# Kernel tuning notes

Hardware: AMD Instinct MI355X
Metric: run time of the kernel (lower is better)

Reference implementation:

```python
import jax, jax.numpy as jnp
import numpy as np

N, E, B, DIM, NF, EF, HID = 16384, 32768, 512, 64, 14, 4, 128

def _p(key, shape, scale):
    return jax.random.normal(key, shape, dtype=jnp.float32) * scale

def setup_inputs() -> dict:
    key = jax.random.key(0)
    ks = jax.random.split(key, 20)
    s = lambda fan: 1.0 / float(np.sqrt(fan))
    z = lambda *sh: jnp.zeros(sh, jnp.float32)
    return {
        "x": jax.random.normal(ks[0], (N, NF), dtype=jnp.float32),
        "edge_index": jax.random.randint(ks[1], (2, E), 0, N),
        "edge_attr": jax.random.uniform(ks[2], (E, EF), dtype=jnp.float32),
        "batch": jnp.sort(jax.random.randint(ks[3], (N,), 0, B)),
        "do_dropout": 0,
        "mlp_drop": 0,
        "lin0_w": _p(ks[4], (NF, DIM), s(NF)), "lin0_b": z(DIM),
        "nn1_w": _p(ks[5], (EF, HID), s(EF)), "nn1_b": z(HID),
        "nn2_w": _p(ks[6], (HID, DIM * DIM), s(HID)), "nn2_b": z(DIM * DIM),
        "root_w": _p(ks[7], (DIM, DIM), s(DIM)), "conv_b": z(DIM),
        "gru_w_ih": _p(ks[8], (3 * DIM, DIM), s(DIM)), "gru_w_hh": _p(ks[9], (3 * DIM, DIM), s(DIM)),
        "gru_b_ih": _p(ks[10], (3 * DIM,), s(DIM)), "gru_b_hh": _p(ks[11], (3 * DIM,), s(DIM)),
        "lstm_w_ih": _p(ks[12], (4 * DIM, 2 * DIM), s(DIM)), "lstm_w_hh": _p(ks[13], (4 * DIM, DIM), s(DIM)),
        "lstm_b_ih": _p(ks[14], (4 * DIM,), s(DIM)), "lstm_b_hh": _p(ks[15], (4 * DIM,), s(DIM)),
        "lin1_w": _p(ks[16], (2 * DIM, DIM), s(2 * DIM)), "lin1_b": z(DIM),
        "lin2_w": _p(ks[17], (DIM, 1), s(DIM)), "lin2_b": z(1),
    }

def _forward(x, edge_attr, lin0_w, lin0_b, nn1_w, nn1_b, nn2_w, nn2_b, root_w, conv_b,
             gru_w_ih, gru_w_hh, gru_b_ih, gru_b_hh,
             lstm_w_ih, lstm_w_hh, lstm_b_ih, lstm_b_hh,
             lin1_w, lin1_b, lin2_w, lin2_b, edge_index, batch):
    src, dst = edge_index[0], edge_index[1]
    out = jax.nn.relu(x @ lin0_w + lin0_b)                      # [N, DIM]
    h = out
    # Edge-conditioned weights (edge_attr is layer-independent -> compute once)
    ew = jax.nn.relu(edge_attr @ nn1_w + nn1_b) @ nn2_w + nn2_b  # [E, DIM*DIM]
    ew = ew.reshape(E, DIM, DIM)
    deg = jax.ops.segment_sum(jnp.ones((E,), jnp.float32), dst, num_segments=N)
    deg = jnp.maximum(deg, 1.0)[:, None]                        # mean aggregation denominator

    def gru_cell(xin, hprev):
        gi = xin @ gru_w_ih.T + gru_b_ih
        gh = hprev @ gru_w_hh.T + gru_b_hh
        ir, iz, inn = jnp.split(gi, 3, axis=-1)
        hr, hz, hn = jnp.split(gh, 3, axis=-1)
        r = jax.nn.sigmoid(ir + hr)
        zg = jax.nn.sigmoid(iz + hz)
        n = jnp.tanh(inn + r * hn)
        return (1.0 - zg) * n + zg * hprev

    for _ in range(3):  # 3 message-passing rounds (structurally fixed)
        msg = jnp.einsum('ed,edf->ef', out[src], ew)            # gather -> per-edge matvec
        agg = jax.ops.segment_sum(msg, dst, num_segments=N) / deg
        m = jax.nn.relu(out @ root_w + agg + conv_b)            # NNConv (root weight + mean aggr)
        h = gru_cell(m, h)
        out = h

    # Set2Set pooling, 3 processing steps
    q_star = jnp.zeros((B, 2 * DIM), jnp.float32)
    hl = jnp.zeros((B, DIM), jnp.float32)
    cl = jnp.zeros((B, DIM), jnp.float32)
    for _ in range(3):
        gates = q_star @ lstm_w_ih.T + lstm_b_ih + hl @ lstm_w_hh.T + lstm_b_hh
        ii, ff, gg, oo = jnp.split(gates, 4, axis=-1)
        cl = jax.nn.sigmoid(ff) * cl + jax.nn.sigmoid(ii) * jnp.tanh(gg)
        hl = jax.nn.sigmoid(oo) * jnp.tanh(cl)
        q = hl                                                  # [B, DIM]
        e = jnp.sum(out * q[batch], axis=-1)                    # [N]
        emax = jax.ops.segment_max(e, batch, num_segments=B)
        ex = jnp.exp(e - emax[batch])
        esum = jnp.maximum(jax.ops.segment_sum(ex, batch, num_segments=B), 1e-16)
        a = ex / esum[batch]                                    # segment softmax
        r = jax.ops.segment_sum(a[:, None] * out, batch, num_segments=B)
        q_star = jnp.concatenate([q, r], axis=-1)               # [B, 2*DIM]

    y = jax.nn.relu(q_star @ lin1_w + lin1_b)
    # dropout flags are False (eval) -> identity
    y = y @ lin2_w + lin2_b
    return y.reshape(-1)                                        # [B]

def reference(x, edge_index, edge_attr, batch, do_dropout, mlp_drop,
              lin0_w, lin0_b, nn1_w, nn1_b, nn2_w, nn2_b, root_w, conv_b,
              gru_w_ih, gru_w_hh, gru_b_ih, gru_b_hh,
              lstm_w_ih, lstm_w_hh, lstm_b_ih, lstm_b_hh,
              lin1_w, lin1_b, lin2_w, lin2_b):
    return _forward(x, edge_attr, lin0_w, lin0_b, nn1_w, nn1_b, nn2_w, nn2_b, root_w, conv_b,
                    gru_w_ih, gru_w_hh, gru_b_ih, gru_b_hh,
                    lstm_w_ih, lstm_w_hh, lstm_b_ih, lstm_b_hh,
                    lin1_w, lin1_b, lin2_w, lin2_b, edge_index, batch)
```

## Files before the change

### kernel.cpp

```cpp
#include <hip/hip_runtime.h>
#include <math.h>

#define N_NODES 16384
#define N_EDGES 32768
#define NGRAPH  512
#define DIM     64
#define NF      14
#define HIDN    128
#define EWCOLS  4096

typedef unsigned short u16;
typedef unsigned int   u32;
typedef __attribute__((ext_vector_type(8))) short bf16x8;
typedef __attribute__((ext_vector_type(4))) float f32x4;
typedef __attribute__((ext_vector_type(4))) u32   u32x4;

__device__ inline float b2f(u16 u){
    unsigned int x = ((unsigned int)u) << 16;
    return __builtin_bit_cast(float, x);
}
__device__ inline u16 f2b(float f){
    unsigned int x = __builtin_bit_cast(unsigned int, f);
    unsigned int r = (x + 0x7FFFu + ((x >> 16) & 1u)) >> 16;
    return (u16)r;
}
__device__ inline float sigf(float x){ return 1.f / (1.f + expf(-x)); }

__global__ __launch_bounds__(256) void k_lin0(const float* __restrict__ x,
        const float* __restrict__ w, const float* __restrict__ b, float* __restrict__ out){
    int n = (blockIdx.x * blockDim.x + threadIdx.x) >> 6;
    int lane = threadIdx.x & 63;
    if (n >= N_NODES) return;
    float xv = (lane < NF) ? x[n * NF + lane] : 0.f;
    float acc = b[lane];
    #pragma unroll
    for (int d = 0; d < NF; ++d){
        float xd = __shfl(xv, d);
        acc += xd * w[d * DIM + lane];
    }
    out[n * DIM + lane] = fmaxf(acc, 0.f);
}

__global__ __launch_bounds__(256) void k_prep(const float* __restrict__ w2,
        const float* __restrict__ lwih, const float* __restrict__ lwhh,
        const float* __restrict__ root, const float* __restrict__ gwih, const float* __restrict__ gwhh,
        u16* __restrict__ w2T, float* __restrict__ wihT, float* __restrict__ whhT,
        u16* __restrict__ rtHi, u16* __restrict__ rtLo,
        u16* __restrict__ wihHi, u16* __restrict__ wihLo,
        u16* __restrict__ whhHi, u16* __restrict__ whhLo){
    int i = blockIdx.x * 256 + threadIdx.x;
    if (i < 524288){
        int k = i >> 12, c = i & 4095;
        w2T[c * HIDN + k] = f2b(w2[i]);
    } else if (i < 557056){
        int i2 = i - 524288;
        int j = i2 >> 7, d = i2 & 127;
        wihT[d * 256 + j] = lwih[i2];
    } else if (i < 573440){
        int i2 = i - 557056;
        int j = i2 >> 6, d = i2 & 63;
        whhT[d * 256 + j] = lwhh[i2];
    } else if (i < 577536){
        int i2 = i - 573440;
        int d = i2 >> 6, j = i2 & 63;
        float v = root[i2]; u16 h = f2b(v);
        rtHi[j * 64 + d] = h; rtLo[j * 64 + d] = f2b(v - b2f(h));
    } else if (i < 589824){
        int k = i - 577536;
        float v = gwih[k]; u16 h = f2b(v);
        wihHi[k] = h; wihLo[k] = f2b(v - b2f(h));
    } else if (i < 602112){
        int k = i - 589824;
        float v = gwhh[k]; u16 h = f2b(v);
        whhHi[k] = h; whhLo[k] = f2b(v - b2f(h));
    }
}

__global__ __launch_bounds__(256) void k_deg(const int* __restrict__ ei, unsigned* __restrict__ degu){
    int e = blockIdx.x * blockDim.x + threadIdx.x;
    if (e < N_EDGES) atomicAdd(&degu[ei[N_EDGES + e]], 1u);
}
__global__ __launch_bounds__(256) void k_dinv(const unsigned* __restrict__ degu, float* __restrict__ dinv){
    int n = blockIdx.x * blockDim.x + threadIdx.x;
    if (n < N_NODES) dinv[n] = 1.f / fmaxf((float)degu[n], 1.f);
}

#define EB   128
#define LDO  68

__global__ __launch_bounds__(512) void k_msg_fused(
        const int* __restrict__ ei, const float* __restrict__ ea,
        const float* __restrict__ w1, const float* __restrict__ b1,
        const u16* __restrict__ w2T, const float* __restrict__ b2,
        const float* __restrict__ out, float* __restrict__ agg)
{
    __shared__ float s_out[EB * LDO];
    __shared__ u16   s_b[2][64 * 128];
    __shared__ float s_b2[EWCOLS];
    __shared__ float s_w1[512];
    __shared__ float s_b1[128];
    int tid = threadIdx.x;
    int e0 = blockIdx.x * EB;

    s_w1[tid] = w1[tid];
    if (tid < 128) s_b1[tid] = b1[tid];
    {
        int base = tid * 8;
        *(float4*)(s_b2 + base)     = *(const float4*)(b2 + base);
        *(float4*)(s_b2 + base + 4) = *(const float4*)(b2 + base + 4);
    }
    {
        int row = tid >> 2, cb = (tid & 3) * 16;
        int s = ei[e0 + row];
        const float4* sp = (const float4*)(out + (size_t)s * DIM + cb);
        float4 v0 = sp[0], v1 = sp[1], v2 = sp[2], v3 = sp[3];
        float* dst = s_out + row * LDO + cb;
        *(float4*)(dst)      = v0;
        *(float4*)(dst + 4)  = v1;
        *(float4*)(dst + 8)  = v2;
        *(float4*)(dst + 12) = v3;
    }
    __syncthreads();

    int wv = tid >> 6, lane = tid & 63;
    int WR = (wv >> 1) * 32, WC = (wv & 1) * 32;
    int lr = lane & 15, lk = (lane >> 4) * 8;

    bf16x8 afr[2][4];
    #pragma unroll
    for (int m = 0; m < 2; ++m){
        int erow = e0 + WR + m*16 + lr;
        float4 av = *(const float4*)(ea + (size_t)erow * 4);
        #pragma unroll
        for (int kk = 0; kk < 4; ++kk){
            bf16x8 t8;
            #pragma unroll
            for (int i = 0; i < 8; ++i){
                int h = kk*32 + lk + i;
                float acc = s_b1[h] + av.x*s_w1[h] + av.y*s_w1[128+h]
                          + av.z*s_w1[256+h] + av.w*s_w1[384+h];
                t8[i] = (short)f2b(fmaxf(acc, 0.f));
            }
            afr[m][kk] = t8;
        }
    }

    int bc = tid >> 3, bs = tid & 7;
    const u32x4* gb = (const u32x4*)w2T;
    u32x4 r0 = gb[((size_t)bc << 4) + bs*2];
    u32x4 r1 = gb[((size_t)bc << 4) + bs*2 + 1];

    f32x4 msg[2][2] = {};
    int swzr = (lr & 7) << 4;
    int swzw = (bc & 7) << 4;
    int crow = (lane >> 4) * 4;

    for (int d = 0; d < 64; ++d){
        char* sw = (char*)s_b[d & 1];
        *(u32x4*)(sw + ((bc*256 + bs*32)      ^ swzw)) = r0;
        *(u32x4*)(sw + ((bc*256 + bs*32 + 16) ^ swzw)) = r1;
        if (d < 63){
            size_t base = ((size_t)(d+1)*64 + bc) << 4;
            r0 = gb[base + bs*2];
            r1 = gb[base + bs*2 + 1];
        }
        __syncthreads();
        const char* sr = (const char*)s_b[d & 1];
        f32x4 ew[2][2] = {};
        #pragma unroll
        for (int kk = 0; kk < 4; ++kk){
            int kb = kk*64 + (lane >> 4) * 16;
            bf16x8 bf0 = *(const bf16x8*)(sr + (((WC + lr)*256 + kb)      ^ swzr));
            bf16x8 bf1 = *(const bf16x8*)(sr + (((WC + 16 + lr)*256 + kb) ^ swzr));
            ew[0][0] = __builtin_amdgcn_mfma_f32_16x16x32_bf16(afr[0][kk], bf0, ew[0][0], 0, 0, 0);
            ew[0][1] = __builtin_amdgcn_mfma_f32_16x16x32_bf16(afr[0][kk], bf1, ew[0][1], 0, 0, 0);
            ew[1][0] = __builtin_amdgcn_mfma_f32_16x16x32_bf16(afr[1][kk], bf0, ew[1][0], 0, 0, 0);
            ew[1][1] = __builtin_amdgcn_mfma_f32_16x16x32_bf16(afr[1][kk], bf1, ew[1][1], 0, 0, 0);
        }
        float b2v0 = s_b2[d*64 + WC + lr];
        float b2v1 = s_b2[d*64 + WC + 16 + lr];
        #pragma unroll
        for (int m = 0; m < 2; ++m){
            #pragma unroll
            for (int r = 0; r < 4; ++r){
                float sc = s_out[(WR + m*16 + crow + r) * LDO + d];
                msg[m][0][r] += sc * (ew[m][0][r] + b2v0);
                msg[m][1][r] += sc * (ew[m][1][r] + b2v1);
            }
        }
    }

    #pragma unroll
    for (int m = 0; m < 2; ++m){
        #pragma unroll
        for (int r = 0; r < 4; ++r){
            int eg = e0 + WR + m*16 + crow + r;
            int dn = ei[N_EDGES + eg];
            atomicAdd(&agg[(size_t)dn * DIM + WC + lr],      msg[m][0][r]);
            atomicAdd(&agg[(size_t)dn * DIM + WC + 16 + lr], msg[m][1][r]);
        }
    }
}

#define LDH 68
__global__ __launch_bounds__(256) void k_update(
        const u16* __restrict__ rtHi, const u16* __restrict__ rtLo,
        const u16* __restrict__ wihHi, const u16* __restrict__ wihLo,
        const u16* __restrict__ whhHi, const u16* __restrict__ whhLo,
        const float* __restrict__ convb, const float* __restrict__ bih,
        const float* __restrict__ bhh,
        const float* __restrict__ agg, const float* __restrict__ dinv,
        float* __restrict__ out)
{
    __shared__ float s_h[64 * LDH];
    __shared__ float s_aux[64 * LDH];
    __shared__ float s_m[64 * LDH];
    int tid = threadIdx.x;
    int n0 = blockIdx.x * 64;

    {
        int row = tid >> 2, cb = (tid & 3) * 16;
        const float4* hp = (const float4*)(out + (size_t)(n0 + row) * DIM + cb);
        const float4* ap = (const float4*)(agg + (size_t)(n0 + row) * DIM + cb);
        float di = dinv[n0 + row];
        #pragma unroll
        for (int q = 0; q < 4; ++q){
            float4 hv = hp[q];
            float4 av = ap[q];
            *(float4*)(s_h + row * LDH + cb + q*4) = hv;
            float4 xv;
            xv.x = av.x * di + convb[cb + q*4 + 0];
            xv.y = av.y * di + convb[cb + q*4 + 1];
            xv.z = av.z * di + convb[cb + q*4 + 2];
            xv.w = av.w * di + convb[cb + q*4 + 3];
            *(float4*)(s_aux + row * LDH + cb + q*4) = xv;
        }
    }
    __syncthreads();

    int wv = tid >> 6, lane = tid & 63;
    int lr = lane & 15, lkb = (lane >> 4) * 8;
    int arow = wv * 16 + lr;

    bf16x8 hHi[2], hLo[2];
    #pragma unroll
    for (int kk = 0; kk < 2; ++kk){
        const float* src = s_h + arow * LDH + kk*32 + lkb;
        bf16x8 hi8, lo8;
        #pragma unroll
        for (int e = 0; e < 8; ++e){
            float v = src[e];
            u16 h = f2b(v);
            hi8[e] = (short)h;
            lo8[e] = (short)f2b(v - b2f(h));
        }
        hHi[kk] = hi8; hLo[kk] = lo8;
    }

    f32x4 c1[4] = {};
    #pragma unroll
    for (int ct = 0; ct < 4; ++ct){
        #pragma unroll
        for (int kk = 0; kk < 2; ++kk){
            int off = (ct*16 + lr) * 64 + kk*32 + lkb;
            bf16x8 bHi = *(const bf16x8*)(rtHi + off);
            bf16x8 bLo = *(const bf16x8*)(rtLo + off);
            c1[ct] = __builtin_amdgcn_mfma_f32_16x16x32_bf16(hHi[kk], bHi, c1[ct], 0, 0, 0);
            c1[ct] = __builtin_amdgcn_mfma_f32_16x16x32_bf16(hLo[kk], bHi, c1[ct], 0, 0, 0);
            c1[ct] = __builtin_amdgcn_mfma_f32_16x16x32_bf16(hHi[kk], bLo, c1[ct], 0, 0, 0);
        }
    }

    int crow = (lane >> 4) * 4;
    #pragma unroll
    for (int ct = 0; ct < 4; ++ct){
        #pragma unroll
        for (int r = 0; r < 4; ++r){
            int row = wv*16 + crow + r;
            int col = ct*16 + lr;
            float m = fmaxf(c1[ct][r] + s_aux[row * LDH + col], 0.f);
            s_m[row * LDH + col] = m;
        }
    }
    __syncthreads();

    bf16x8 mHi[2], mLo[2];
    #pragma unroll
    for (int kk = 0; kk < 2; ++kk){
        const float* src = s_m + arow * LDH + kk*32 + lkb;
        bf16x8 hi8, lo8;
        #pragma unroll
        for (int e = 0; e < 8; ++e){
            float v = src[e];
            u16 h = f2b(v);
            hi8[e] = (short)h;
            lo8[e] = (short)f2b(v - b2f(h));
        }
        mHi[kk] = hi8; mLo[kk] = lo8;
    }

    f32x4 gi[12] = {}, gh[12] = {};
    #pragma unroll
    for (int ct = 0; ct < 12; ++ct){
        #pragma unroll
        for (int kk = 0; kk < 2; ++kk){
            int off = (ct*16 + lr) * 64 + kk*32 + lkb;
            bf16x8 biH = *(const bf16x8*)(wihHi + off);
            bf16x8 biL = *(const bf16x8*)(wihLo + off);
            gi[ct] = __builtin_amdgcn_mfma_f32_16x16x32_bf16(mHi[kk], biH, gi[ct], 0, 0, 0);
            gi[ct] = __builtin_amdgcn_mfma_f32_16x16x32_bf16(mLo[kk], biH, gi[ct], 0, 0, 0);
            gi[ct] = __builtin_amdgcn_mfma_f32_16x16x32_bf16(mHi[kk], biL, gi[ct], 0, 0, 0);
            bf16x8 bhH = *(const bf16x8*)(whhHi + off);
            bf16x8 bhL = *(const bf16x8*)(whhLo + off);
            gh[ct] = __builtin_amdgcn_mfma_f32_16x16x32_bf16(hHi[kk], bhH, gh[ct], 0, 0, 0);
            gh[ct] = __builtin_amdgcn_mfma_f32_16x16x32_bf16(hLo[kk], bhH, gh[ct], 0, 0, 0);
            gh[ct] = __builtin_amdgcn_mfma_f32_16x16x32_bf16(hHi[kk], bhL, gh[ct], 0, 0, 0);
        }
    }

    #pragma unroll
    for (int ct = 0; ct < 4; ++ct){
        int col = ct*16 + lr;
        float br_i = bih[col],       br_h = bhh[col];
        float bz_i = bih[64 + col],  bz_h = bhh[64 + col];
        float bn_i = bih[128 + col], bn_h = bhh[128 + col];
        #pragma unroll
        for (int r = 0; r < 4; ++r){
            int row = wv*16 + crow + r;
            float rg = sigf(gi[ct][r] + br_i + gh[ct][r] + br_h);
            float zg = sigf(gi[ct+4][r] + bz_i + gh[ct+4][r] + bz_h);
            float ng = tanhf(gi[ct+8][r] + bn_i + rg * (gh[ct+8][r] + bn_h));
            float h  = s_h[row * LDH + col];
            s_aux[row * LDH + col] = (1.f - zg) * ng + zg * h;
        }
    }
    __syncthreads();

    {
        int row = tid >> 2, cb = (tid & 3) * 16;
        #pragma unroll
        for (int q = 0; q < 4; ++q)
            *(float4*)(out + (size_t)(n0 + row) * DIM + cb + q*4) =
                *(const float4*)(s_aux + row * LDH + cb + q*4);
    }
}

__global__ __launch_bounds__(256) void k_s2s(
        const float* __restrict__ out, const int* __restrict__ batch,
        const float* __restrict__ wihT, const float* __restrict__ lbih,
        const float* __restrict__ whhT, const float* __restrict__ lbhh,
        const float* __restrict__ l1w, const float* __restrict__ l1b,
        const float* __restrict__ l2w, const float* __restrict__ l2b,
        float* __restrict__ y)
{
    __shared__ float s_q[128];
    __shared__ float s_hc[128];
    __shared__ float s_g[256];
    __shared__ float s_rw[256];
    __shared__ float s_sw[8];
    __shared__ int   s_rng[2];
    int g = blockIdx.x, tid = threadIdx.x;
    if (tid < 2){
        int target = g + tid;
        int lo = 0, hi = N_NODES;
        while (lo < hi){ int mid = (lo + hi) >> 1; if (batch[mid] < target) lo = mid + 1; else hi = mid; }
        s_rng[tid] = lo;
    }
    if (tid < 128){ s_q[tid] = 0.f; s_hc[tid] = 0.f; }
    __syncthreads();
    int s0 = s_rng[0], s1 = s_rng[1];
    int wv = tid >> 6, lane = tid & 63;

    for (int step = 0; step < 3; ++step){
        float acc = lbih[tid] + lbhh[tid];
        #pragma unroll 8
        for (int d = 0; d < 128; ++d) acc += s_q[d] * wihT[d * 256 + tid];
        #pragma unroll 8
        for (int d = 0; d < 64;  ++d) acc += s_hc[d] * whhT[d * 256 + tid];
        s_g[tid] = acc;
        __syncthreads();
        if (tid < 64){
            float c = sigf(s_g[64 + tid]) * s_hc[64 + tid] + sigf(s_g[tid]) * tanhf(s_g[128 + tid]);
            float h = sigf(s_g[192 + tid]) * tanhf(c);
            s_hc[tid] = h; s_hc[64 + tid] = c;
            s_q[tid] = h;
        }
        __syncthreads();
        float q = s_hc[lane];
        float emx = -3.4e38f;
        for (int n = s0 + wv; n < s1; n += 4){
            float v = out[(size_t)n * DIM + lane] * q;
            #pragma unroll
            for (int off = 32; off; off >>= 1) v += __shfl_xor(v, off);
            emx = fmaxf(emx, v);
        }
        if (lane == 0) s_sw[wv] = emx;
        __syncthreads();
        float gmax = fmaxf(fmaxf(s_sw[0], s_sw[1]), fmaxf(s_sw[2], s_sw[3]));
        float rl = 0.f, ss = 0.f;
        for (int n = s0 + wv; n < s1; n += 4){
            float o = out[(size_t)n * DIM + lane];
            float v = o * q;
            #pragma unroll
            for (int off = 32; off; off >>= 1) v += __shfl_xor(v, off);
            float ex = expf(v - gmax);
            rl += ex * o;
            ss += ex;
        }
        s_rw[wv * 64 + lane] = rl;
        if (lane == 0) s_sw[4 + wv] = ss;
        __syncthreads();
        if (tid < 64){
            float r = s_rw[tid] + s_rw[64 + tid] + s_rw[128 + tid] + s_rw[192 + tid];
            float S = fmaxf(s_sw[4] + s_sw[5] + s_sw[6] + s_sw[7], 1e-16f);
            s_q[64 + tid] = r / S;
        }
        __syncthreads();
    }
    if (wv == 0){
        float acc = l1b[lane];
        #pragma unroll 8
        for (int d = 0; d < 128; ++d) acc += s_q[d] * l1w[d * 64 + lane];
        float h = fmaxf(acc, 0.f);
        float p = h * l2w[lane];
        #pragma unroll
        for (int off = 32; off; off >>= 1) p += __shfl_down(p, off);
        if (lane == 0) y[g] = p + l2b[0];
    }
}

extern "C" void kernel_launch(void* const* d_in, const int* in_sizes, int n_in,
                              void* d_out, int out_size, void* d_ws, size_t ws_size,
                              hipStream_t stream){
    const float* x      = (const float*)d_in[0];
    const int*   ei     = (const int*)d_in[1];
    const float* ea     = (const float*)d_in[2];
    const int*   batch  = (const int*)d_in[3];
    const float* lin0_w = (const float*)d_in[6];
    const float* lin0_b = (const float*)d_in[7];
    const float* nn1_w  = (const float*)d_in[8];
    const float* nn1_b  = (const float*)d_in[9];
    const float* nn2_w  = (const float*)d_in[10];
    const float* nn2_b  = (const float*)d_in[11];
    const float* root_w = (const float*)d_in[12];
    const float* conv_b = (const float*)d_in[13];
    const float* gwih   = (const float*)d_in[14];
    const float* gwhh   = (const float*)d_in[15];
    const float* gbih   = (const float*)d_in[16];
    const float* gbhh   = (const float*)d_in[17];
    const float* lwih   = (const float*)d_in[18];
    const float* lwhh   = (const float*)d_in[19];
    const float* lbih   = (const float*)d_in[20];
    const float* lbhh   = (const float*)d_in[21];
    const float* l1w    = (const float*)d_in[22];
    const float* l1b    = (const float*)d_in[23];
    const float* l2w    = (const float*)d_in[24];
    const float* l2b    = (const float*)d_in[25];
    float* y = (float*)d_out;

    char* p = (char*)d_ws;
    float* out   = (float*)p;    p += (size_t)N_NODES * DIM * 4;
    float* agg   = (float*)p;    p += (size_t)N_NODES * DIM * 4;
    u16* w2T     = (u16*)p;      p += (size_t)EWCOLS * HIDN * 2;
    float* wihT  = (float*)p;    p += 128 * 256 * 4;
    float* whhT  = (float*)p;    p += 64 * 256 * 4;
    u16* rtHi    = (u16*)p;      p += 4096 * 2;
    u16* rtLo    = (u16*)p;      p += 4096 * 2;
    u16* wihHi   = (u16*)p;      p += 12288 * 2;
    u16* wihLo   = (u16*)p;      p += 12288 * 2;
    u16* whhHi   = (u16*)p;      p += 12288 * 2;
    u16* whhLo   = (u16*)p;      p += 12288 * 2;
    unsigned* degu = (unsigned*)p; p += N_NODES * 4;
    float* dinv  = (float*)p;    p += N_NODES * 4;

    if ((size_t)(p - (char*)d_ws) > ws_size) return;

    hipMemsetAsync(degu, 0, N_NODES * 4, stream);

    k_prep<<<2352, 256, 0, stream>>>(nn2_w, lwih, lwhh, root_w, gwih, gwhh,
                w2T, wihT, whhT, rtHi, rtLo, wihHi, wihLo, whhHi, whhLo);
    k_lin0<<<N_NODES / 4, 256, 0, stream>>>(x, lin0_w, lin0_b, out);
    k_deg <<<N_EDGES / 256, 256, 0, stream>>>(ei, degu);
    k_dinv<<<N_NODES / 256, 256, 0, stream>>>(degu, dinv);

    for (int r = 0; r < 3; ++r){
        hipMemsetAsync(agg, 0, (size_t)N_NODES * DIM * 4, stream);
        k_msg_fused<<<N_EDGES / EB, 512, 0, stream>>>(ei, ea, nn1_w, nn1_b, w2T, nn2_b, out, agg);
        k_update   <<<N_NODES / 64, 256, 0, stream>>>(rtHi, rtLo, wihHi, wihLo, whhHi, whhLo,
                        conv_b, gbih, gbhh, agg, dinv, out);
    }

    k_s2s<<<NGRAPH, 256, 0, stream>>>(out, batch, wihT, lbih, whhT, lbhh,
                l1w, l1b, l2w, l2b, y);
}
```

Baseline: 300.9 us.

## Stream edge-weight tiles via direct global-to-LDS loads and hoist bias term

The per-edge weight tile loads in the fused message kernel now use global_load_lds, which writes straight into double-buffered shared memory instead of staging through registers. This removes the register round trip and the explicit LDS stores, with a single barrier per step. The gathered node features are stored transposed so each step reads them as one vector load. The b2 bias contribution is moved out of the main loop into a separate pass that reads b2 from global memory, which removes the bias shared-memory buffer and its per-step adds. The risks are that correctness now depends on the placement and semantics of the async LDS loads, and that the transposed scalar stores may cause bank conflicts.

```diff
diff --git a/kernel.cpp b/kernel.cpp
--- a/kernel.cpp
+++ b/kernel.cpp
@@ -14,6 +14,8 @@
 typedef __attribute__((ext_vector_type(8))) short bf16x8;
 typedef __attribute__((ext_vector_type(4))) float f32x4;
 typedef __attribute__((ext_vector_type(4))) u32   u32x4;
+typedef __attribute__((address_space(1))) const u32 as1_u32;
+typedef __attribute__((address_space(3))) u32       as3_u32;
 
 __device__ inline float b2f(u16 u){
     unsigned int x = ((unsigned int)u) << 16;
@@ -86,7 +88,7 @@
 }
 
 #define EB   128
-#define LDO  68
+#define LDT_O 132
 
 __global__ __launch_bounds__(512) void k_msg_fused(
         const int* __restrict__ ei, const float* __restrict__ ea,
@@ -94,37 +96,45 @@
         const u16* __restrict__ w2T, const float* __restrict__ b2,
         const float* __restrict__ out, float* __restrict__ agg)
 {
-    __shared__ float s_out[EB * LDO];
+    __shared__ float s_oT[64 * LDT_O];
     __shared__ u16   s_b[2][64 * 128];
-    __shared__ float s_b2[EWCOLS];
     __shared__ float s_w1[512];
     __shared__ float s_b1[128];
     int tid = threadIdx.x;
     int e0 = blockIdx.x * EB;
+    int wv = tid >> 6, lane = tid & 63;
+
+    int c0 = (wv*2)     * 4 + (lane >> 4);
+    int c1 = (wv*2 + 1) * 4 + (lane >> 4);
+    int o0 = ((((lane & 15) << 4) ^ ((c0 & 7) << 4)) >> 1);
+    int o1 = ((((lane & 15) << 4) ^ ((c1 & 7) << 4)) >> 1);
+    const u16* g0 = w2T + c0 * HIDN + o0;
+    const u16* g1 = w2T + c1 * HIDN + o1;
+
+    __builtin_amdgcn_global_load_lds((as1_u32*)g0,
+        (as3_u32*)((char*)s_b[0] + (wv*2)*1024), 16, 0, 0);
+    __builtin_amdgcn_global_load_lds((as1_u32*)g1,
+        (as3_u32*)((char*)s_b[0] + (wv*2+1)*1024), 16, 0, 0);
 
     s_w1[tid] = w1[tid];
     if (tid < 128) s_b1[tid] = b1[tid];
     {
-        int base = tid * 8;
-        *(float4*)(s_b2 + base)     = *(const float4*)(b2 + base);
-        *(float4*)(s_b2 + base + 4) = *(const float4*)(b2 + base + 4);
-    }
-    {
-        int row = tid >> 2, cb = (tid & 3) * 16;
+        int row = tid >> 2, q = tid & 3;
         int s = ei[e0 + row];
-        const float4* sp = (const float4*)(out + (size_t)s * DIM + cb);
+        const float4* sp = (const float4*)(out + (size_t)s * DIM + q * 16);
         float4 v0 = sp[0], v1 = sp[1], v2 = sp[2], v3 = sp[3];
-        float* dst = s_out + row * LDO + cb;
-        *(float4*)(dst)      = v0;
-        *(float4*)(dst + 4)  = v1;
-        *(float4*)(dst + 8)  = v2;
-        *(float4*)(dst + 12) = v3;
+        float* op = s_oT + (q * 16) * LDT_O + row;
+        op[0*LDT_O]=v0.x;  op[1*LDT_O]=v0.y;  op[2*LDT_O]=v0.z;  op[3*LDT_O]=v0.w;
+        op[4*LDT_O]=v1.x;  op[5*LDT_O]=v1.y;  op[6*LDT_O]=v1.z;  op[7*LDT_O]=v1.w;
+        op[8*LDT_O]=v2.x;  op[9*LDT_O]=v2.y;  op[10*LDT_O]=v2.z; op[11*LDT_O]=v2.w;
+        op[12*LDT_O]=v3.x; op[13*LDT_O]=v3.y; op[14*LDT_O]=v3.z; op[15*LDT_O]=v3.w;
     }
     __syncthreads();
 
-    int wv = tid >> 6, lane = tid & 63;
     int WR = (wv >> 1) * 32, WC = (wv & 1) * 32;
     int lr = lane & 15, lk = (lane >> 4) * 8;
+    int crow = (lane >> 4) * 4;
+    int swzr = (lr & 7) << 4;
 
     bf16x8 afr[2][4];
     #pragma unroll
@@ -145,48 +155,54 @@
         }
     }
 
-    int bc = tid >> 3, bs = tid & 7;
-    const u32x4* gb = (const u32x4*)w2T;
-    u32x4 r0 = gb[((size_t)bc << 4) + bs*2];
-    u32x4 r1 = gb[((size_t)bc << 4) + bs*2 + 1];
-
     f32x4 msg[2][2] = {};
-    int swzr = (lr & 7) << 4;
-    int swzw = (bc & 7) << 4;
-    int crow = (lane >> 4) * 4;
 
     for (int d = 0; d < 64; ++d){
-        char* sw = (char*)s_b[d & 1];
-        *(u32x4*)(sw + ((bc*256 + bs*32)      ^ swzw)) = r0;
-        *(u32x4*)(sw + ((bc*256 + bs*32 + 16) ^ swzw)) = r1;
-        if (d < 63){
-            size_t base = ((size_t)(d+1)*64 + bc) << 4;
-            r0 = gb[base + bs*2];
-            r1 = gb[base + bs*2 + 1];
-        }
-        __syncthreads();
+        if (d + 1 < 64){
+            size_t pb = (size_t)(d + 1) * 8192;
+            char* dst = (char*)s_b[(d + 1) & 1];
+            __builtin_amdgcn_global_load_lds((as1_u32*)(g0 + pb),
+                (as3_u32*)(dst + (wv*2)*1024), 16, 0, 0);
+            __builtin_amdgcn_global_load_lds((as1_u32*)(g1 + pb),
+                (as3_u32*)(dst + (wv*2+1)*1024), 16, 0, 0);
+        }
         const char* sr = (const char*)s_b[d & 1];
-        f32x4 ew[2][2] = {};
+        f32x4 ew00 = {}, ew01 = {}, ew10 = {}, ew11 = {};
         #pragma unroll
         for (int kk = 0; kk < 4; ++kk){
             int kb = kk*64 + (lane >> 4) * 16;
             bf16x8 bf0 = *(const bf16x8*)(sr + (((WC + lr)*256 + kb)      ^ swzr));
             bf16x8 bf1 = *(const bf16x8*)(sr + (((WC + 16 + lr)*256 + kb) ^ swzr));
-            ew[0][0] = __builtin_amdgcn_mfma_f32_16x16x32_bf16(afr[0][kk], bf0, ew[0][0], 0, 0, 0);
-            ew[0][1] = __builtin_amdgcn_mfma_f32_16x16x32_bf16(afr[0][kk], bf1, ew[0][1], 0, 0, 0);
-            ew[1][0] = __builtin_amdgcn_mfma_f32_16x16x32_bf16(afr[1][kk], bf0, ew[1][0], 0, 0, 0);
-            ew[1][1] = __builtin_amdgcn_mfma_f32_16x16x32_bf16(afr[1][kk], bf1, ew[1][1], 0, 0, 0);
-        }
-        float b2v0 = s_b2[d*64 + WC + lr];
-        float b2v1 = s_b2[d*64 + WC + 16 + lr];
-        #pragma unroll
-        for (int m = 0; m < 2; ++m){
-            #pragma unroll
-            for (int r = 0; r < 4; ++r){
-                float sc = s_out[(WR + m*16 + crow + r) * LDO + d];
-                msg[m][0][r] += sc * (ew[m][0][r] + b2v0);
-                msg[m][1][r] += sc * (ew[m][1][r] + b2v1);
-            }
+            ew00 = __builtin_amdgcn_mfma_f32_16x16x32_bf16(afr[0][kk], bf0, ew00, 0, 0, 0);
+            ew01 = __builtin_amdgcn_mfma_f32_16x16x32_bf16(afr[0][kk], bf1, ew01, 0, 0, 0);
+            ew10 = __builtin_amdgcn_mfma_f32_16x16x32_bf16(afr[1][kk], bf0, ew10, 0, 0, 0);
+            ew11 = __builtin_amdgcn_mfma_f32_16x16x32_bf16(afr[1][kk], bf1, ew11, 0, 0, 0);
+        }
+        f32x4 sc0 = *(const f32x4*)(s_oT + d * LDT_O + WR + crow);
+        f32x4 sc1 = *(const f32x4*)(s_oT + d * LDT_O + WR + 16 + crow);
+        #pragma unroll
+        for (int r = 0; r < 4; ++r){
+            msg[0][0][r] += sc0[r] * ew00[r];
+            msg[0][1][r] += sc0[r] * ew01[r];
+            msg[1][0][r] += sc1[r] * ew10[r];
+            msg[1][1][r] += sc1[r] * ew11[r];
+        }
+        __syncthreads();
+    }
+
+    int f0 = WC + lr;
+    #pragma unroll 8
+    for (int dd = 0; dd < 64; ++dd){
+        float bv0 = b2[dd*64 + f0];
+        float bv1 = b2[dd*64 + f0 + 16];
+        f32x4 sc0 = *(const f32x4*)(s_oT + dd * LDT_O + WR + crow);
+        f32x4 sc1 = *(const f32x4*)(s_oT + dd * LDT_O + WR + 16 + crow);
+        #pragma unroll
+        for (int r = 0; r < 4; ++r){
+            msg[0][0][r] += sc0[r] * bv0;
+            msg[0][1][r] += sc0[r] * bv1;
+            msg[1][0][r] += sc1[r] * bv0;
+            msg[1][1][r] += sc1[r] * bv1;
         }
     }
 
```

Result: slower. 357.7 us (+18.9%).

## Split message kernel over input-dimension halves to raise occupancy

Applied to the files above, without the earlier changes.

The fused edge-message kernel now launches a second grid dimension, with each block handling 32 of the 64 input features (d) for its 128 edges, so grid size doubles from 256 to 512 blocks. Shared memory is shrunk by staging only half of each source row and by dropping the shared nn2 bias copy in favour of direct global loads, and launch bounds request 4 blocks per SM. The edge MLP hidden layer is recomputed in both halves and twice as many atomicAdds hit agg, trading redundant work and atomic traffic for better GPU fill on a small grid.

```diff
diff --git a/kernel.cpp b/kernel.cpp
--- a/kernel.cpp
+++ b/kernel.cpp
@@ -86,39 +86,37 @@
 }
 
 #define EB   128
-#define LDO  68
-
-__global__ __launch_bounds__(512) void k_msg_fused(
+#define LDO2 36
+
+__global__ __launch_bounds__(512, 4) void k_msg_fused(
         const int* __restrict__ ei, const float* __restrict__ ea,
         const float* __restrict__ w1, const float* __restrict__ b1,
         const u16* __restrict__ w2T, const float* __restrict__ b2,
         const float* __restrict__ out, float* __restrict__ agg)
 {
-    __shared__ float s_out[EB * LDO];
+    __shared__ float s_out[EB * LDO2];
     __shared__ u16   s_b[2][64 * 128];
-    __shared__ float s_b2[EWCOLS];
     __shared__ float s_w1[512];
     __shared__ float s_b1[128];
     int tid = threadIdx.x;
     int e0 = blockIdx.x * EB;
+    int d0 = blockIdx.y * 32;
+
+    int bc = tid >> 3, bs = tid & 7;
+    const u32x4* gb = (const u32x4*)w2T;
+    u32x4 r0 = gb[(((size_t)d0 * 64 + bc) << 4) + bs*2];
+    u32x4 r1 = gb[(((size_t)d0 * 64 + bc) << 4) + bs*2 + 1];
 
     s_w1[tid] = w1[tid];
     if (tid < 128) s_b1[tid] = b1[tid];
     {
-        int base = tid * 8;
-        *(float4*)(s_b2 + base)     = *(const float4*)(b2 + base);
-        *(float4*)(s_b2 + base + 4) = *(const float4*)(b2 + base + 4);
-    }
-    {
-        int row = tid >> 2, cb = (tid & 3) * 16;
+        int row = tid >> 2, q = tid & 3;
         int s = ei[e0 + row];
-        const float4* sp = (const float4*)(out + (size_t)s * DIM + cb);
-        float4 v0 = sp[0], v1 = sp[1], v2 = sp[2], v3 = sp[3];
-        float* dst = s_out + row * LDO + cb;
-        *(float4*)(dst)      = v0;
-        *(float4*)(dst + 4)  = v1;
-        *(float4*)(dst + 8)  = v2;
-        *(float4*)(dst + 12) = v3;
+        const float4* sp = (const float4*)(out + (size_t)s * DIM + d0 + q * 8);
+        float4 v0 = sp[0], v1 = sp[1];
+        float* dst = s_out + row * LDO2 + q * 8;
+        *(float4*)(dst)     = v0;
+        *(float4*)(dst + 4) = v1;
     }
     __syncthreads();
 
@@ -145,48 +143,44 @@
         }
     }
 
-    int bc = tid >> 3, bs = tid & 7;
-    const u32x4* gb = (const u32x4*)w2T;
-    u32x4 r0 = gb[((size_t)bc << 4) + bs*2];
-    u32x4 r1 = gb[((size_t)bc << 4) + bs*2 + 1];
-
     f32x4 msg[2][2] = {};
     int swzr = (lr & 7) << 4;
     int swzw = (bc & 7) << 4;
     int crow = (lane >> 4) * 4;
 
-    for (int d = 0; d < 64; ++d){
+    for (int d = 0; d < 32; ++d){
         char* sw = (char*)s_b[d & 1];
         *(u32x4*)(sw + ((bc*256 + bs*32)      ^ swzw)) = r0;
         *(u32x4*)(sw + ((bc*256 + bs*32 + 16) ^ swzw)) = r1;
-        if (d < 63){
-            size_t base = ((size_t)(d+1)*64 + bc) << 4;
+        if (d < 31){
+            size_t base = ((size_t)(d0 + d + 1) * 64 + bc) << 4;
             r0 = gb[base + bs*2];
             r1 = gb[base + bs*2 + 1];
         }
         __syncthreads();
         const char* sr = (const char*)s_b[d & 1];
-        f32x4 ew[2][2] = {};
+        f32x4 ew00 = {}, ew01 = {}, ew10 = {}, ew11 = {};
         #pragma unroll
         for (int kk = 0; kk < 4; ++kk){
             int kb = kk*64 + (lane >> 4) * 16;
             bf16x8 bf0 = *(const bf16x8*)(sr + (((WC + lr)*256 + kb)      ^ swzr));
             bf16x8 bf1 = *(const bf16x8*)(sr + (((WC + 16 + lr)*256 + kb) ^ swzr));
-            ew[0][0] = __builtin_amdgcn_mfma_f32_16x16x32_bf16(afr[0][kk], bf0, ew[0][0], 0, 0, 0);
-            ew[0][1] = __builtin_amdgcn_mfma_f32_16x16x32_bf16(afr[0][kk], bf1, ew[0][1], 0, 0, 0);
-            ew[1][0] = __builtin_amdgcn_mfma_f32_16x16x32_bf16(afr[1][kk], bf0, ew[1][0], 0, 0, 0);
-            ew[1][1] = __builtin_amdgcn_mfma_f32_16x16x32_bf16(afr[1][kk], bf1, ew[1][1], 0, 0, 0);
-        }
-        float b2v0 = s_b2[d*64 + WC + lr];
-        float b2v1 = s_b2[d*64 + WC + 16 + lr];
-        #pragma unroll
-        for (int m = 0; m < 2; ++m){
-            #pragma unroll
-            for (int r = 0; r < 4; ++r){
-                float sc = s_out[(WR + m*16 + crow + r) * LDO + d];
-                msg[m][0][r] += sc * (ew[m][0][r] + b2v0);
-                msg[m][1][r] += sc * (ew[m][1][r] + b2v1);
-            }
+            ew00 = __builtin_amdgcn_mfma_f32_16x16x32_bf16(afr[0][kk], bf0, ew00, 0, 0, 0);
+            ew01 = __builtin_amdgcn_mfma_f32_16x16x32_bf16(afr[0][kk], bf1, ew01, 0, 0, 0);
+            ew10 = __builtin_amdgcn_mfma_f32_16x16x32_bf16(afr[1][kk], bf0, ew10, 0, 0, 0);
+            ew11 = __builtin_amdgcn_mfma_f32_16x16x32_bf16(afr[1][kk], bf1, ew11, 0, 0, 0);
+        }
+        int f0g = (d0 + d) * 64 + WC + lr;
+        float b2v0 = b2[f0g];
+        float b2v1 = b2[f0g + 16];
+        #pragma unroll
+        for (int r = 0; r < 4; ++r){
+            float sc0 = s_out[(WR + crow + r) * LDO2 + d];
+            float sc1 = s_out[(WR + 16 + crow + r) * LDO2 + d];
+            msg[0][0][r] += sc0 * (ew00[r] + b2v0);
+            msg[0][1][r] += sc0 * (ew01[r] + b2v1);
+            msg[1][0][r] += sc1 * (ew10[r] + b2v0);
+            msg[1][1][r] += sc1 * (ew11[r] + b2v1);
         }
     }
 
@@ -485,7 +479,7 @@
 
     for (int r = 0; r < 3; ++r){
         hipMemsetAsync(agg, 0, (size_t)N_NODES * DIM * 4, stream);
-        k_msg_fused<<<N_EDGES / EB, 512, 0, stream>>>(ei, ea, nn1_w, nn1_b, w2T, nn2_b, out, agg);
+        k_msg_fused<<<dim3(N_EDGES / EB, 2), 512, 0, stream>>>(ei, ea, nn1_w, nn1_b, w2T, nn2_b, out, agg);
         k_update   <<<N_NODES / 64, 256, 0, stream>>>(rtHi, rtLo, wihHi, wihLo, whhHi, whhLo,
                         conv_b, gbih, gbhh, agg, dinv, out);
     }
```

Result: slower. 578.9 us (+92.4%).
